# Kernel tuning notes

Hardware: AMD Instinct MI355X
Metric: run time of the kernel (lower is better)

Reference implementation:

```python
import jax, jax.numpy as jnp
import numpy as np

B, T, D, H, L, NS = 256, 256, 128, 512, 3, 24  # batch, seq, input_dim, n_units, num_layers, n_steps


def setup_inputs() -> dict:
    key = jax.random.key(0)
    ks = jax.random.split(key, 1 + 4 * L + 2)
    inp = {"x": jax.random.normal(ks[0], (B, T, D), dtype=jnp.float32)}
    s = 1.0 / np.sqrt(H)  # PyTorch GRU init scale
    i = 1
    for l in range(L):
        din = D if l == 0 else H
        inp[f"w_ih{l}"] = jax.random.uniform(ks[i], (3 * H, din), jnp.float32, -s, s); i += 1
        inp[f"w_hh{l}"] = jax.random.uniform(ks[i], (3 * H, H), jnp.float32, -s, s); i += 1
        inp[f"b_ih{l}"] = jax.random.uniform(ks[i], (3 * H,), jnp.float32, -s, s); i += 1
        inp[f"b_hh{l}"] = jax.random.uniform(ks[i], (3 * H,), jnp.float32, -s, s); i += 1
    sf = 1.0 / np.sqrt(H)
    inp["fc_w"] = jax.random.uniform(ks[i], (NS, H), jnp.float32, -sf, sf)
    inp["fc_b"] = jax.random.uniform(ks[i + 1], (NS,), jnp.float32, -sf, sf)
    return inp


def gru_layer(x, w_ih, w_hh, b_ih, b_hh):
    # x: [B, T, Din] -> [B, T, H]. Gate order (PyTorch): r, z, n.
    gx = jnp.einsum('btd,gd->btg', x, w_ih) + b_ih  # precompute input gates: [B, T, 3H]
    Hd = w_hh.shape[1]

    def step(h, gx_t):
        gh = h @ w_hh.T + b_hh  # [B, 3H]
        xr, xz, xn = jnp.split(gx_t, 3, axis=-1)
        hr, hz, hn = jnp.split(gh, 3, axis=-1)
        r = jax.nn.sigmoid(xr + hr)
        z = jax.nn.sigmoid(xz + hz)
        n = jnp.tanh(xn + r * hn)
        h_new = (1.0 - z) * n + z * h
        return h_new, h_new

    h0 = jnp.zeros((x.shape[0], Hd), dtype=x.dtype)
    _, ys = jax.lax.scan(step, h0, jnp.swapaxes(gx, 0, 1))  # scan over time
    return jnp.swapaxes(ys, 0, 1)  # [B, T, H]


def reference(x, w_ih0, w_hh0, b_ih0, b_hh0, w_ih1, w_hh1, b_ih1, b_hh1,
              w_ih2, w_hh2, b_ih2, b_hh2, fc_w, fc_b):
    h = gru_layer(x, w_ih0, w_hh0, b_ih0, b_hh0)
    h = gru_layer(h, w_ih1, w_hh1, b_ih1, b_hh1)
    h = gru_layer(h, w_ih2, w_hh2, b_ih2, b_hh2)
    return h[:, -1, :] @ fc_w.T + fc_b  # [B, NS]
```

## Files before the change

### kernel.cpp

```cpp
#include <hip/hip_runtime.h>
#include <cstdint>
#include <cstddef>

typedef _Float16 f16;
typedef _Float16 f16x8 __attribute__((ext_vector_type(8)));
typedef float f32x4 __attribute__((ext_vector_type(4)));
typedef unsigned int u32;
typedef unsigned short u16;
typedef u32 u32x4 __attribute__((ext_vector_type(4)));

#define NB 256
#define NT 256
#define ND 128
#define NH 512
#define NG 1536
#define NOUT 24
#define PL (NB * NH)

__device__ __forceinline__ float fsig(float x) {
  float e = __expf(-x);
  return __fdividef(1.0f, 1.0f + e);
}
__device__ __forceinline__ float ftanh(float x) {
  float ax = __builtin_fabsf(x);
  float e = __expf(-2.0f * ax);
  float t = __fdividef(1.0f - e, 1.0f + e);
  return __builtin_copysignf(t, x);
}

__global__ void k_f32_to_f16(const float* __restrict__ in, f16* __restrict__ out, int n) {
  int stride = gridDim.x * blockDim.x;
  for (int i = blockIdx.x * blockDim.x + threadIdx.x; i < n; i += stride)
    out[i] = (f16)in[i];
}

__device__ __forceinline__ void gl16(const f16* g, f16* l) {
  __builtin_amdgcn_global_load_lds(
      (const __attribute__((address_space(1))) u32*)(const void*)g,
      (__attribute__((address_space(3))) u32*)(void*)l, 16, 0, 0);
}

template <int K>
__global__ __launch_bounds__(256) void k_gemm2(
    const f16* __restrict__ A, const f16* __restrict__ W,
    const float* __restrict__ bias, f16* __restrict__ gx, int t0, int tsh) {
  __shared__ f16 As[128 * 32];
  __shared__ f16 Bs[128 * 32];
  const int tid = threadIdx.x;
  const int wave = tid >> 6, lane = tid & 63;
  const int wm = wave >> 1, wn = wave & 1;
  const int m0 = blockIdx.x * 128;
  const int n0 = blockIdx.y * 128;
  const int tmask = (1 << tsh) - 1;

  const int r0 = tid >> 2;
  const int swzs = (r0 >> 1) & 3;
  const int csrc = ((tid & 3) ^ swzs) * 8;
  const int ga0 = m0 + r0, ga1 = m0 + r0 + 64;
  const int gr0 = ((ga0 >> tsh) << 8) + t0 + (ga0 & tmask);
  const int gr1 = ((ga1 >> tsh) << 8) + t0 + (ga1 & tmask);
  const f16* a0 = A + (size_t)gr0 * K + csrc;
  const f16* a1 = A + (size_t)gr1 * K + csrc;
  const f16* b0 = W + (size_t)(n0 + r0) * K + csrc;
  const f16* b1 = W + (size_t)(n0 + r0 + 64) * K + csrc;
  f16* asb = As + wave * 512;
  f16* bsb = Bs + wave * 512;

  const int lr = lane & 15;
  const int kg = lane >> 4;
  const int swzr = ((lr >> 1) & 3);
  const int koff = (kg ^ swzr) * 8;

  f32x4 acc[4][4];
#pragma unroll
  for (int i = 0; i < 4; i++)
#pragma unroll
    for (int j = 0; j < 4; j++) acc[i][j] = (f32x4){0.f, 0.f, 0.f, 0.f};

  for (int k0 = 0; k0 < K; k0 += 32) {
    gl16(a0 + k0, asb);
    gl16(a1 + k0, asb + 2048);
    gl16(b0 + k0, bsb);
    gl16(b1 + k0, bsb + 2048);
    asm volatile("s_waitcnt vmcnt(0)" ::: "memory");
    __syncthreads();
    f16x8 af[4], bf[4];
#pragma unroll
    for (int i = 0; i < 4; i++)
      af[i] = *(const f16x8*)(As + (wm * 64 + i * 16 + lr) * 32 + koff);
#pragma unroll
    for (int j = 0; j < 4; j++)
      bf[j] = *(const f16x8*)(Bs + (wn * 64 + j * 16 + lr) * 32 + koff);
#pragma unroll
    for (int i = 0; i < 4; i++)
#pragma unroll
      for (int j = 0; j < 4; j++)
        acc[i][j] = __builtin_amdgcn_mfma_f32_16x16x32_f16(af[i], bf[j], acc[i][j], 0, 0, 0);
    __syncthreads();
  }
  const int rowb = (lane >> 4) * 4;
#pragma unroll
  for (int j = 0; j < 4; j++) {
    int col = n0 + wn * 64 + j * 16 + lr;
    float bv = bias[col];
#pragma unroll
    for (int i = 0; i < 4; i++) {
      int row = m0 + wm * 64 + i * 16 + rowb;
#pragma unroll
      for (int rr = 0; rr < 4; rr++)
        gx[(size_t)(row + rr) * NG + col] = (f16)(acc[i][j][rr] + bv);
    }
  }
}

#define ISSUE4K(qarr, kkb)                                               \
  _Pragma("unroll") for (int u_ = 0; u_ < 4; u_++) {                     \
    const u32* pp_ = hq + (kkb + u_) * 32 + lkh * 8;                     \
    asm volatile("global_load_dwordx4 %0, %1, off sc0 sc1"               \
                 : "=v"(qarr[2 * u_]) : "v"(pp_));                       \
    asm volatile("global_load_dwordx4 %0, %1, off sc0 sc1"               \
                 : "=v"(qarr[2 * u_ + 1]) : "v"(pp_ + 4));               \
  }

#define CONS4K(qarr, kkb, nb0)                                                       \
  _Pragma("unroll") for (int u_ = 0; u_ < 4; u_++) {                                 \
    const int kk_ = kkb + u_;                                                        \
    union { u32 w[4]; f16x8 v; } AH_, AL_;                                           \
    AH_.w[0] = __builtin_amdgcn_perm(qarr[2*u_][1],   qarr[2*u_][0],   0x05040100u); \
    AH_.w[1] = __builtin_amdgcn_perm(qarr[2*u_][3],   qarr[2*u_][2],   0x05040100u); \
    AH_.w[2] = __builtin_amdgcn_perm(qarr[2*u_+1][1], qarr[2*u_+1][0], 0x05040100u); \
    AH_.w[3] = __builtin_amdgcn_perm(qarr[2*u_+1][3], qarr[2*u_+1][2], 0x05040100u); \
    AL_.w[0] = __builtin_amdgcn_perm(qarr[2*u_][1],   qarr[2*u_][0],   0x07060302u); \
    AL_.w[1] = __builtin_amdgcn_perm(qarr[2*u_][3],   qarr[2*u_][2],   0x07060302u); \
    AL_.w[2] = __builtin_amdgcn_perm(qarr[2*u_+1][1], qarr[2*u_+1][0], 0x07060302u); \
    AL_.w[3] = __builtin_amdgcn_perm(qarr[2*u_+1][3], qarr[2*u_+1][2], 0x07060302u); \
    const int co_ = (((kk_ * 4 + lkh) ^ swz) << 3);                                  \
    f16x8 bro_ = *(const f16x8*)(wro_ + co_);                                        \
    f16x8 bzo_ = *(const f16x8*)(wzo_ + co_);                                        \
    f16x8 brx_ = *(const f16x8*)(wrx_ + co_);                                        \
    f16x8 bzx_ = *(const f16x8*)(wzx_ + co_);                                        \
    f16x8 bno_ = bnO[nb0 + u_];                                                      \
    f16x8 bnx_ = bnX[nb0 + u_];                                                      \
    aRo = __builtin_amdgcn_mfma_f32_16x16x32_f16(AH_.v, bro_, aRo, 0, 0, 0);         \
    aZo = __builtin_amdgcn_mfma_f32_16x16x32_f16(AH_.v, bzo_, aZo, 0, 0, 0);         \
    aNo = __builtin_amdgcn_mfma_f32_16x16x32_f16(AH_.v, bno_, aNo, 0, 0, 0);         \
    aRx = __builtin_amdgcn_mfma_f32_16x16x32_f16(AH_.v, brx_, aRx, 0, 0, 0);         \
    aZx = __builtin_amdgcn_mfma_f32_16x16x32_f16(AH_.v, bzx_, aZx, 0, 0, 0);         \
    aNx = __builtin_amdgcn_mfma_f32_16x16x32_f16(AH_.v, bnx_, aNx, 0, 0, 0);         \
    aRo = __builtin_amdgcn_mfma_f32_16x16x32_f16(AL_.v, bro_, aRo, 0, 0, 0);         \
    aZo = __builtin_amdgcn_mfma_f32_16x16x32_f16(AL_.v, bzo_, aZo, 0, 0, 0);         \
    aNo = __builtin_amdgcn_mfma_f32_16x16x32_f16(AL_.v, bno_, aNo, 0, 0, 0);         \
    aRx = __builtin_amdgcn_mfma_f32_16x16x32_f16(AL_.v, brx_, aRx, 0, 0, 0);         \
    aZx = __builtin_amdgcn_mfma_f32_16x16x32_f16(AL_.v, bzx_, aZx, 0, 0, 0);         \
    aNx = __builtin_amdgcn_mfma_f32_16x16x32_f16(AL_.v, bnx_, aNx, 0, 0, 0);         \
  }

struct RecUnit {
  const f16* gx; const f16* whh; const float* bhh;
  u32* exq; u32* fl; int t0; int bar_base;
};

__global__ __launch_bounds__(256, 2) void k_rec(
    RecUnit u0, RecUnit u1, RecUnit u2, f16* __restrict__ h, int Tc) {
  __shared__ f16 wlds[64 * 512];
  __shared__ float plds[2][2][64][12];
  RecUnit U = u0;
  const int ui = blockIdx.x >> 7;
  if (ui == 1) U = u1;
  if (ui == 2) U = u2;
  const int bid = blockIdx.x & 127;
  const f16* __restrict__ gx = U.gx;
  u32* __restrict__ exq = U.exq;
  const int t0 = U.t0, bar_base = U.bar_base;
  const int tid = threadIdx.x;
  const int g = bid >> 4;
  const int cs = bid & 15;
  const int b0 = g * 32, c0 = cs * 32;
  const int lane = tid & 63, wave = tid >> 6;
  const int wm = wave >> 1, ks = wave & 1;
  const int lr = lane & 15, lkh = lane >> 4;
  const int first = (t0 == 0) ? 1 : 0;
  const int jo = ks * 16 + lr;
  const int jx = (1 - ks) * 16 + lr;
  const int ks8 = ks * 8;

  f16x8 bnO[8], bnX[8];
  {
    const f16* wb = U.whh + (size_t)(2 * NH + c0) * NH + (size_t)ks8 * 32 + lkh * 8;
    const f16* wO = wb + (size_t)jo * NH;
    const f16* wX = wb + (size_t)jx * NH;
#pragma unroll
    for (int i = 0; i < 8; i++) {
      bnO[i] = *(const f16x8*)(wO + i * 32);
      bnX[i] = *(const f16x8*)(wX + i * 32);
    }
  }
  for (int idx = tid; idx < 64 * 64; idx += 256) {
    int lrw = idx >> 6, c = idx & 63;
    int grow = (lrw >> 5) * NH + c0 + (lrw & 31);
    f16x8 v = *(const f16x8*)(U.whh + (size_t)grow * NH + c * 8);
    *(f16x8*)(wlds + lrw * 512 + ((c ^ (lrw & 7)) << 3)) = v;
  }
  __syncthreads();

  const int j = c0 + jo;
  const float bh_r = U.bhh[j], bh_z = U.bhh[NH + j], bh_n = U.bhh[2 * NH + j];
  const int arow = b0 + wm * 16 + lr;
  const int rowbase = b0 + wm * 16 + lkh * 4;
  const int swz = lr & 7;
  const f16* wro_ = wlds + jo * 512;
  const f16* wzo_ = wlds + (32 + jo) * 512;
  const f16* wrx_ = wlds + jx * 512;
  const f16* wzx_ = wlds + (32 + jx) * 512;
  u32* myflag = U.fl + g * 64 + cs;
  u32* gflags = U.fl + g * 64;
  const int pl = lane & 15;

  union PK2 { u32 u; f16 hh[2]; };

  float hold[4];
  if (first) {
#pragma unroll
    for (int r = 0; r < 4; r++) hold[r] = 0.f;
  } else {
#pragma unroll
    for (int r = 0; r < 4; r++) {
      PK2 pk;
      pk.u = __hip_atomic_load(exq + (size_t)(rowbase + r) * NH + j,
                               __ATOMIC_RELAXED, __HIP_MEMORY_SCOPE_AGENT);
      hold[r] = (float)pk.hh[0] + (float)pk.hh[1];
    }
  }

  float xr[4], xz[4], xn[4];
#pragma unroll
  for (int r = 0; r < 4; r++) {
    const f16* gp = gx + ((size_t)(rowbase + r) * Tc) * NG + j;
    xr[r] = (float)gp[0]; xz[r] = (float)gp[NH]; xn[r] = (float)gp[2 * NH];
  }

  int cur = 0;
  for (int t = 0; t < Tc; t++) {
    f32x4 aRo = {0.f, 0.f, 0.f, 0.f}, aZo = {0.f, 0.f, 0.f, 0.f}, aNo = {0.f, 0.f, 0.f, 0.f};
    f32x4 aRx = {0.f, 0.f, 0.f, 0.f}, aZx = {0.f, 0.f, 0.f, 0.f}, aNx = {0.f, 0.f, 0.f, 0.f};
    if (t > 0 || !first) {
      const u32* hq = exq + (size_t)cur * PL + (size_t)arow * NH;
      u32x4 q0[8], q1[8];
      ISSUE4K(q0, ks8);
      ISSUE4K(q1, ks8 + 4);
      asm volatile("s_waitcnt vmcnt(8)" ::: "memory");
      __builtin_amdgcn_sched_barrier(0);
      CONS4K(q0, ks8, 0);
      asm volatile("s_waitcnt vmcnt(0)" ::: "memory");
      __builtin_amdgcn_sched_barrier(0);
      CONS4K(q1, ks8 + 4, 4);
      float* ps = &plds[wm][ks][lane][0];
#pragma unroll
      for (int i = 0; i < 4; i++) {
        ps[i] = aRx[i]; ps[4 + i] = aZx[i]; ps[8 + i] = aNx[i];
      }
      __syncthreads();
      const float* pr = &plds[wm][1 - ks][lane][0];
#pragma unroll
      for (int i = 0; i < 4; i++) {
        aRo[i] += pr[i]; aZo[i] += pr[4 + i]; aNo[i] += pr[8 + i];
      }
    }
    u32* outq = exq + (size_t)(cur ^ 1) * PL;
    f16 hhi_s[4];
#pragma unroll
    for (int r = 0; r < 4; r++) {
      float rg = fsig(xr[r] + aRo[r] + bh_r);
      float zg = fsig(xz[r] + aZo[r] + bh_z);
      float ng = ftanh(xn[r] + rg * (aNo[r] + bh_n));
      float hnew = ng + zg * (hold[r] - ng);
      hold[r] = hnew;
      PK2 pk;
      pk.hh[0] = (f16)hnew;
      pk.hh[1] = (f16)(hnew - (float)pk.hh[0]);
      hhi_s[r] = pk.hh[0];
      __hip_atomic_store(outq + (size_t)(rowbase + r) * NH + j, pk.u,
                         __ATOMIC_RELAXED, __HIP_MEMORY_SCOPE_AGENT);
    }
    if (t < Tc - 1) {
      asm volatile("s_waitcnt vmcnt(0)" ::: "memory");
      __syncthreads();
      if (tid == 0)
        __hip_atomic_store(myflag, (u32)(bar_base + t + 1),
                           __ATOMIC_RELAXED, __HIP_MEMORY_SCOPE_AGENT);
#pragma unroll
      for (int r = 0; r < 4; r++)
        h[((size_t)(rowbase + r) * NT + (t0 + t)) * NH + j] = hhi_s[r];
#pragma unroll
      for (int r = 0; r < 4; r++) {
        const f16* gp = gx + ((size_t)(rowbase + r) * Tc + (t + 1)) * NG + j;
        xr[r] = (float)gp[0]; xz[r] = (float)gp[NH]; xn[r] = (float)gp[2 * NH];
      }
      asm volatile("" ::: "memory");
      const u32 target = (u32)(bar_base + t + 1);
      for (;;) {
        u32 v = __hip_atomic_load(gflags + pl,
                                  __ATOMIC_RELAXED, __HIP_MEMORY_SCOPE_AGENT);
        if (__all(v >= target)) break;
        __builtin_amdgcn_s_sleep(1);
      }
      asm volatile("" ::: "memory");
    } else {
#pragma unroll
      for (int r = 0; r < 4; r++)
        h[((size_t)(rowbase + r) * NT + (t0 + t)) * NH + j] = hhi_s[r];
    }
    cur ^= 1;
  }
}

__global__ void k_fc(const f16* __restrict__ h, const float* __restrict__ fcw,
                     const float* __restrict__ fcb, float* __restrict__ out) {
  int b = blockIdx.x;
  int lane = threadIdx.x;
  __shared__ float hrow[NH];
  for (int k = lane; k < NH; k += 64)
    hrow[k] = (float)h[((size_t)b * NT + (NT - 1)) * NH + k];
  __syncthreads();
  for (int o = 0; o < NOUT; o++) {
    float sm = 0.f;
    for (int k = lane; k < NH; k += 64) sm += hrow[k] * fcw[o * NH + k];
#pragma unroll
    for (int off = 32; off; off >>= 1) sm += __shfl_down(sm, off);
    if (lane == 0) out[b * NOUT + o] = sm + fcb[o];
  }
}

extern "C" void kernel_launch(void* const* d_in, const int* in_sizes, int n_in,
                              void* d_out, int out_size, void* d_ws, size_t ws_size,
                              hipStream_t stream) {
  (void)in_sizes; (void)n_in; (void)out_size;
  const float* x = (const float*)d_in[0];
  const float* w_ih[3] = {(const float*)d_in[1], (const float*)d_in[5], (const float*)d_in[9]};
  const float* w_hh[3] = {(const float*)d_in[2], (const float*)d_in[6], (const float*)d_in[10]};
  const float* b_ih[3] = {(const float*)d_in[3], (const float*)d_in[7], (const float*)d_in[11]};
  const float* b_hh[3] = {(const float*)d_in[4], (const float*)d_in[8], (const float*)d_in[12]};
  const float* fcw = (const float*)d_in[13];
  const float* fcb = (const float*)d_in[14];

  const size_t fixed = 32768 +
                       ((size_t)NG * ND + 2 * (size_t)NG * NH) * 2  +
                       3 * (size_t)NG * NH * 2  +
                       (size_t)NB * NT * ND * 2  +
                       (size_t)NB * NT * NH * 2  +
                       3 * (size_t)2 * PL * 4 ;
  int Tc = 64;
  while (Tc > 16 && fixed + 3 * ((size_t)NB * Tc * NG * 2) > ws_size) Tc >>= 1;
  const int nc = NT / Tc;
  int tsh = 0;
  while ((1 << tsh) < Tc) tsh++;

  char* p = (char*)d_ws;
  size_t off = 0;
  u32* ctrl = (u32*)(p + off); off += 32768;
  f16* wih_f[3]; f16* whh_f[3];
  const int wih_sz[3] = {NG * ND, NG * NH, NG * NH};
  for (int l = 0; l < 3; l++) {
    wih_f[l] = (f16*)(p + off); off += (size_t)wih_sz[l] * 2;
    whh_f[l] = (f16*)(p + off); off += (size_t)NG * NH * 2;
  }
  f16* xf16 = (f16*)(p + off); off += (size_t)NB * NT * ND * 2;
  f16* h = (f16*)(p + off); off += (size_t)NB * NT * NH * 2;
  u32* exq[3];
  for (int l = 0; l < 3; l++) {
    exq[l] = (u32*)(p + off); off += (size_t)2 * PL * 4;
  }
  f16* gxbuf[3];
  for (int s = 0; s < 3; s++) {
    gxbuf[s] = (f16*)(p + off); off += (size_t)NB * Tc * NG * 2;
  }

  hipMemsetAsync(ctrl, 0, 32768, stream);

  auto conv = [&](const float* src, f16* dst, int n) {
    int blocks = (n + 1023) / 1024; if (blocks > 2048) blocks = 2048;
    k_f32_to_f16<<<dim3(blocks), dim3(256), 0, stream>>>(src, dst, n);
  };
  conv(x, xf16, NB * NT * ND);
  for (int l = 0; l < 3; l++) {
    conv(w_ih[l], wih_f[l], wih_sz[l]);
    conv(w_hh[l], whh_f[l], NG * NH);
  }

  const int mblocks = (NB * Tc) / 128;

  for (int d = 0; d < 3 + nc - 1; d++) {
    int pl_[3], pc_[3], np = 0;
    for (int l = 0; l < 3; l++) {
      int c = d - l;
      if (c < 0 || c >= nc) continue;
      pl_[np] = l; pc_[np] = c; np++;
    }
    if (np == 0) continue;
    for (int s = 0; s < np; s++) {
      int l = pl_[s], c = pc_[s];
      if (l == 0)
        k_gemm2<ND><<<dim3(mblocks, 12), dim3(256), 0, stream>>>(
            xf16, wih_f[0], b_ih[0], gxbuf[s], c * Tc, tsh);
      else
        k_gemm2<NH><<<dim3(mblocks, 12), dim3(256), 0, stream>>>(
            h, wih_f[l], b_ih[l], gxbuf[s], c * Tc, tsh);
    }
    RecUnit us[3];
    for (int s = 0; s < np; s++) {
      int l = pl_[s], c = pc_[s];
      us[s].gx = gxbuf[s];
      us[s].whh = whh_f[l];
      us[s].bhh = b_hh[l];
      us[s].exq = exq[l];
      us[s].fl = ctrl + l * 512;
      us[s].t0 = c * Tc;
      us[s].bar_base = c * (Tc - 1);
    }
    for (int s = np; s < 3; s++) us[s] = us[0];
    k_rec<<<dim3(np * 128), dim3(256), 0, stream>>>(us[0], us[1], us[2], h, Tc);
  }
  k_fc<<<dim3(NB), dim3(64), 0, stream>>>(h, fcw, fcb, (float*)d_out);
}
```

Measured before the change: 2.556 ms.

## Fuse fp32-to-fp16 conversions into one vectorized kernel and deepen GEMM K-tile

The seven separate fp32-to-fp16 conversion launches are replaced by a single kernel that converts all tensors with float4 loads and f16x4 stores. This cuts launch overhead and widens memory accesses. The input-projection GEMM now stages 64-wide K tiles in LDS instead of 32-wide, with an 8-way XOR swizzle, which halves the number of barrier and wait rounds per output tile. The cost is doubled shared-memory use per block, which may lower occupancy.

New measurement: 2.646 ms. +3.5%, slower.

```diff
diff --git a/kernel.cpp b/kernel.cpp
--- a/kernel.cpp
+++ b/kernel.cpp
@@ -3,6 +3,7 @@
 #include <cstddef>
 
 typedef _Float16 f16;
+typedef _Float16 f16x4 __attribute__((ext_vector_type(4)));
 typedef _Float16 f16x8 __attribute__((ext_vector_type(8)));
 typedef float f32x4 __attribute__((ext_vector_type(4)));
 typedef unsigned int u32;
@@ -28,10 +29,27 @@
   return __builtin_copysignf(t, x);
 }
 
-__global__ void k_f32_to_f16(const float* __restrict__ in, f16* __restrict__ out, int n) {
-  int stride = gridDim.x * blockDim.x;
-  for (int i = blockIdx.x * blockDim.x + threadIdx.x; i < n; i += stride)
-    out[i] = (f16)in[i];
+__global__ void k_conv_all(
+    const float* s0, f16* d0, int n0, const float* s1, f16* d1, int n1,
+    const float* s2, f16* d2, int n2, const float* s3, f16* d3, int n3,
+    const float* s4, f16* d4, int n4, const float* s5, f16* d5, int n5,
+    const float* s6, f16* d6, int n6) {
+  const int stride = gridDim.x * blockDim.x;
+  const int t = blockIdx.x * blockDim.x + threadIdx.x;
+#define CONVSEG(S, D, N)                                        \
+  for (int i = t; i < (N) / 4; i += stride) {                   \
+    float4 v = *(const float4*)((S) + (size_t)i * 4);           \
+    f16x4 o = {(f16)v.x, (f16)v.y, (f16)v.z, (f16)v.w};        \
+    *(f16x4*)((D) + (size_t)i * 4) = o;                         \
+  }
+  CONVSEG(s0, d0, n0)
+  CONVSEG(s1, d1, n1)
+  CONVSEG(s2, d2, n2)
+  CONVSEG(s3, d3, n3)
+  CONVSEG(s4, d4, n4)
+  CONVSEG(s5, d5, n5)
+  CONVSEG(s6, d6, n6)
+#undef CONVSEG
 }
 
 __device__ __forceinline__ void gl16(const f16* g, f16* l) {
@@ -44,8 +62,8 @@
 __global__ __launch_bounds__(256) void k_gemm2(
     const f16* __restrict__ A, const f16* __restrict__ W,
     const float* __restrict__ bias, f16* __restrict__ gx, int t0, int tsh) {
-  __shared__ f16 As[128 * 32];
-  __shared__ f16 Bs[128 * 32];
+  __shared__ f16 As[128 * 64];
+  __shared__ f16 Bs[128 * 64];
   const int tid = threadIdx.x;
   const int wave = tid >> 6, lane = tid & 63;
   const int wm = wave >> 1, wn = wave & 1;
@@ -53,23 +71,23 @@
   const int n0 = blockIdx.y * 128;
   const int tmask = (1 << tsh) - 1;
 
-  const int r0 = tid >> 2;
-  const int swzs = (r0 >> 1) & 3;
-  const int csrc = ((tid & 3) ^ swzs) * 8;
-  const int ga0 = m0 + r0, ga1 = m0 + r0 + 64;
-  const int gr0 = ((ga0 >> tsh) << 8) + t0 + (ga0 & tmask);
-  const int gr1 = ((ga1 >> tsh) << 8) + t0 + (ga1 & tmask);
-  const f16* a0 = A + (size_t)gr0 * K + csrc;
-  const f16* a1 = A + (size_t)gr1 * K + csrc;
-  const f16* b0 = W + (size_t)(n0 + r0) * K + csrc;
-  const f16* b1 = W + (size_t)(n0 + r0 + 64) * K + csrc;
-  f16* asb = As + wave * 512;
-  f16* bsb = Bs + wave * 512;
+  const int r0 = tid >> 3;
+  const int csrc = ((tid & 7) ^ (r0 & 7)) * 8;
+  const f16* ap[4];
+  const f16* bp[4];
+#pragma unroll
+  for (int q = 0; q < 4; q++) {
+    int ga = m0 + r0 + q * 32;
+    int gr = ((ga >> tsh) << 8) + t0 + (ga & tmask);
+    ap[q] = A + (size_t)gr * K + csrc;
+    bp[q] = W + (size_t)(n0 + r0 + q * 32) * K + csrc;
+  }
+  f16* asw = As + wave * 512;
+  f16* bsw = Bs + wave * 512;
 
   const int lr = lane & 15;
   const int kg = lane >> 4;
-  const int swzr = ((lr >> 1) & 3);
-  const int koff = (kg ^ swzr) * 8;
+  const int sw = lr & 7;
 
   f32x4 acc[4][4];
 #pragma unroll
@@ -77,25 +95,30 @@
 #pragma unroll
     for (int j = 0; j < 4; j++) acc[i][j] = (f32x4){0.f, 0.f, 0.f, 0.f};
 
-  for (int k0 = 0; k0 < K; k0 += 32) {
-    gl16(a0 + k0, asb);
-    gl16(a1 + k0, asb + 2048);
-    gl16(b0 + k0, bsb);
-    gl16(b1 + k0, bsb + 2048);
+  for (int k0 = 0; k0 < K; k0 += 64) {
+#pragma unroll
+    for (int q = 0; q < 4; q++) {
+      gl16(ap[q] + k0, asw + q * 2048);
+      gl16(bp[q] + k0, bsw + q * 2048);
+    }
     asm volatile("s_waitcnt vmcnt(0)" ::: "memory");
     __syncthreads();
-    f16x8 af[4], bf[4];
-#pragma unroll
-    for (int i = 0; i < 4; i++)
-      af[i] = *(const f16x8*)(As + (wm * 64 + i * 16 + lr) * 32 + koff);
-#pragma unroll
-    for (int j = 0; j < 4; j++)
-      bf[j] = *(const f16x8*)(Bs + (wn * 64 + j * 16 + lr) * 32 + koff);
-#pragma unroll
-    for (int i = 0; i < 4; i++)
+#pragma unroll
+    for (int s = 0; s < 2; s++) {
+      const int koff = ((s * 4 + kg) ^ sw) * 8;
+      f16x8 af[4], bf[4];
+#pragma unroll
+      for (int i = 0; i < 4; i++)
+        af[i] = *(const f16x8*)(As + (wm * 64 + i * 16 + lr) * 64 + koff);
 #pragma unroll
       for (int j = 0; j < 4; j++)
-        acc[i][j] = __builtin_amdgcn_mfma_f32_16x16x32_f16(af[i], bf[j], acc[i][j], 0, 0, 0);
+        bf[j] = *(const f16x8*)(Bs + (wn * 64 + j * 16 + lr) * 64 + koff);
+#pragma unroll
+      for (int i = 0; i < 4; i++)
+#pragma unroll
+        for (int j = 0; j < 4; j++)
+          acc[i][j] = __builtin_amdgcn_mfma_f32_16x16x32_f16(af[i], bf[j], acc[i][j], 0, 0, 0);
+    }
     __syncthreads();
   }
   const int rowb = (lane >> 4) * 4;
@@ -377,15 +400,11 @@
 
   hipMemsetAsync(ctrl, 0, 32768, stream);
 
-  auto conv = [&](const float* src, f16* dst, int n) {
-    int blocks = (n + 1023) / 1024; if (blocks > 2048) blocks = 2048;
-    k_f32_to_f16<<<dim3(blocks), dim3(256), 0, stream>>>(src, dst, n);
-  };
-  conv(x, xf16, NB * NT * ND);
-  for (int l = 0; l < 3; l++) {
-    conv(w_ih[l], wih_f[l], wih_sz[l]);
-    conv(w_hh[l], whh_f[l], NG * NH);
-  }
+  k_conv_all<<<dim3(2048), dim3(256), 0, stream>>>(
+      x, xf16, NB * NT * ND,
+      w_ih[0], wih_f[0], wih_sz[0], w_hh[0], whh_f[0], NG * NH,
+      w_ih[1], wih_f[1], wih_sz[1], w_hh[1], whh_f[1], NG * NH,
+      w_ih[2], wih_f[2], wih_sz[2], w_hh[2], whh_f[2], NG * NH);
 
   const int mblocks = (NB * Tc) / 128;
 
```
